# Kernel tuning notes

Hardware: AMD Instinct MI355X
Metric: run time of the kernel (lower is better)

The kernel has to match this reference:

```python
import math
import jax, jax.numpy as jnp
import numpy as np

N_EMBD = 448
NUM_HEADS = 8


def setup_inputs() -> dict:
    key = jax.random.key(0)
    ks = jax.random.split(key, 6)
    B, T, C = 4, 2048, N_EMBD
    x = jax.random.normal(ks[0], (B, T, C), dtype=jnp.float32)
    # Linear weights stored as [in, out]; y = x @ W (bias-free for q/k/v).
    s = 1.0 / math.sqrt(C)
    Wq = jax.random.normal(ks[1], (C, C), dtype=jnp.float32) * s
    Wk = jax.random.normal(ks[2], (C, C), dtype=jnp.float32) * s
    Wv = jax.random.normal(ks[3], (C, C), dtype=jnp.float32) * s
    Wp = jax.random.normal(ks[4], (C, C), dtype=jnp.float32) * s
    bp = jax.random.normal(ks[5], (C,), dtype=jnp.float32) * 0.01
    return {"x": x, "Wq": Wq, "Wk": Wk, "Wv": Wv, "Wp": Wp, "bp": bp}


def reference(x, Wq, Wk, Wv, Wp, bp):
    B, T, C = x.shape
    H = NUM_HEADS
    d = C // H
    # Projections, split into heads: [B, H, T, d]
    q = (x @ Wq).reshape(B, T, H, d).transpose(0, 2, 1, 3)
    k = (x @ Wk).reshape(B, T, H, d).transpose(0, 2, 1, 3)
    v = (x @ Wv).reshape(B, T, H, d).transpose(0, 2, 1, 3)
    # NOTE: original scales by 1/sqrt(C) (full embed dim), not 1/sqrt(head_dim).
    scale = 1.0 / math.sqrt(C)
    wei = jnp.einsum("bhtd,bhsd->bhts", q, k) * scale  # [B, H, T, T]
    causal = jnp.tril(jnp.ones((T, T), dtype=bool))
    wei = jnp.where(causal, wei, -jnp.inf)
    wei = jax.nn.softmax(wei, axis=-1)
    # dropout(p=0.2) is identity in eval mode
    out = jnp.einsum("bhts,bhsd->bhtd", wei, v)  # [B, H, T, d]
    out = out.transpose(0, 2, 1, 3).reshape(B, T, C)
    return out @ Wp + bp
```

## Files before the change

kernel.cpp:

```cpp
#include <hip/hip_runtime.h>
#include <math.h>

#define NB 4
#define NT 2048
#define NC 448
#define NH 8
#define ND 56
#define NM (NB * NT)
#define SCALE 0.04724555912615705f

typedef __attribute__((ext_vector_type(8))) short bf16x8;
typedef __attribute__((ext_vector_type(4))) float f32x4;

__device__ __forceinline__ unsigned short f2bf(float f) {
    unsigned u = __float_as_uint(f);
    u += 0x7fffu + ((u >> 16) & 1u);
    return (unsigned short)(u >> 16);
}
__device__ __forceinline__ float bf2f(unsigned short h) {
    return __uint_as_float(((unsigned)h) << 16);
}

__device__ __forceinline__ void gl_lds16(const unsigned short* g, unsigned short* l) {
    __builtin_amdgcn_global_load_lds(
        (const __attribute__((address_space(1))) unsigned int*)g,
        (__attribute__((address_space(3))) unsigned int*)l,
        16, 0, 0);
}

__device__ __forceinline__ int sw_slot(int row, int u) {
    return row * 4 + (u ^ ((row >> 1) & 3));
}

__global__ __launch_bounds__(256) void conv_x_kernel(
    const float* __restrict__ x, unsigned short* __restrict__ xh,
    unsigned short* __restrict__ xl)
{
    const size_t i4 = ((size_t)blockIdx.x * 256 + threadIdx.x) * 4;
    const float4 v = *reinterpret_cast<const float4*>(x + i4);
    ushort4 h, l;
    h.x = f2bf(v.x); l.x = f2bf(v.x - bf2f(h.x));
    h.y = f2bf(v.y); l.y = f2bf(v.y - bf2f(h.y));
    h.z = f2bf(v.z); l.z = f2bf(v.z - bf2f(h.z));
    h.w = f2bf(v.w); l.w = f2bf(v.w - bf2f(h.w));
    *reinterpret_cast<ushort4*>(xh + i4) = h;
    *reinterpret_cast<ushort4*>(xl + i4) = l;
}

__global__ __launch_bounds__(256) void conv_wt_kernel(
    const float* __restrict__ Wq, const float* __restrict__ Wk,
    const float* __restrict__ Wv, const float* __restrict__ Wp,
    unsigned short* __restrict__ wth, unsigned short* __restrict__ wtl)
{
    const int z = blockIdx.z;
    const float* __restrict__ W =
        (z == 0) ? Wq : ((z == 1) ? Wk : ((z == 2) ? Wv : Wp));
    unsigned short* __restrict__ oh = wth + (size_t)z * NC * NC;
    unsigned short* __restrict__ ol = wtl + (size_t)z * NC * NC;

    __shared__ float t[32][33];
    const int tx = threadIdx.x & 31;
    const int ty = threadIdx.x >> 5;
    const int x0 = blockIdx.x * 32;
    const int y0 = blockIdx.y * 32;

    #pragma unroll
    for (int i = 0; i < 4; ++i)
        t[ty + i * 8][tx] = W[(size_t)(y0 + ty + i * 8) * NC + x0 + tx];
    __syncthreads();
    #pragma unroll
    for (int i = 0; i < 4; ++i) {
        const int n = x0 + ty + i * 8;
        const int k = y0 + tx;
        const float v = t[tx][ty + i * 8];
        const unsigned short h = f2bf(v);
        oh[(size_t)n * NC + k] = h;
        ol[(size_t)n * NC + k] = f2bf(v - bf2f(h));
    }
}

__global__ __launch_bounds__(256) void qkv_mfma_kernel(
    const unsigned short* __restrict__ xh, const unsigned short* __restrict__ xl,
    const unsigned short* __restrict__ wth, const unsigned short* __restrict__ wtl,
    unsigned short* __restrict__ qo, unsigned short* __restrict__ ko,
    unsigned short* __restrict__ vo)
{
    const int z = blockIdx.z;
    const unsigned short* __restrict__ BTH = wth + (size_t)z * NC * NC;
    const unsigned short* __restrict__ BTL = wtl + (size_t)z * NC * NC;

    __shared__ unsigned short Ah[128 * 32], Al[128 * 32];
    __shared__ unsigned short Bh[64 * 32],  Bl[64 * 32];
    const int tid = threadIdx.x;
    const int l  = tid & 63, w = tid >> 6;
    const int lg = l >> 4,  lr = l & 15;
    const int wr = w >> 1,  wc = w & 1;
    const int rowBase = blockIdx.y * 128;
    const int colBase = blockIdx.x * 64;

    f32x4 acc[4][2];
    #pragma unroll
    for (int m = 0; m < 4; ++m)
        #pragma unroll
        for (int n = 0; n < 2; ++n) acc[m][n] = (f32x4){0.f, 0.f, 0.f, 0.f};

    for (int k0 = 0; k0 < NC; k0 += 32) {
        __syncthreads();
        #pragma unroll
        for (int i = 0; i < 2; ++i) {
            const int p   = w * 64 + 256 * i + l;
            const int row = p >> 2, ps = p & 3;
            const int u   = ps ^ ((row >> 1) & 3);
            const size_t src = (size_t)(rowBase + row) * NC + k0 + u * 8;
            const int dst = (w * 64 + 256 * i) * 8;
            gl_lds16(xh + src, Ah + dst);
            gl_lds16(xl + src, Al + dst);
        }
        {
            const int p   = w * 64 + l;
            const int row = p >> 2, ps = p & 3;
            const int u   = ps ^ ((row >> 1) & 3);
            const size_t src = (size_t)(colBase + row) * NC + k0 + u * 8;
            gl_lds16(BTH + src, Bh + w * 512);
            gl_lds16(BTL + src, Bl + w * 512);
        }
        __syncthreads();

        bf16x8 a_h[4], a_l[4], b_h[2], b_l[2];
        #pragma unroll
        for (int m = 0; m < 4; ++m) {
            const int row = wr * 64 + m * 16 + lr;
            const int s   = sw_slot(row, lg) * 8;
            a_h[m] = *reinterpret_cast<const bf16x8*>(Ah + s);
            a_l[m] = *reinterpret_cast<const bf16x8*>(Al + s);
        }
        #pragma unroll
        for (int n = 0; n < 2; ++n) {
            const int row = wc * 32 + n * 16 + lr;
            const int s   = sw_slot(row, lg) * 8;
            b_h[n] = *reinterpret_cast<const bf16x8*>(Bh + s);
            b_l[n] = *reinterpret_cast<const bf16x8*>(Bl + s);
        }
        #pragma unroll
        for (int m = 0; m < 4; ++m)
            #pragma unroll
            for (int n = 0; n < 2; ++n) {
                acc[m][n] = __builtin_amdgcn_mfma_f32_16x16x32_bf16(
                    a_h[m], b_h[n], acc[m][n], 0, 0, 0);
                acc[m][n] = __builtin_amdgcn_mfma_f32_16x16x32_bf16(
                    a_h[m], b_l[n], acc[m][n], 0, 0, 0);
                acc[m][n] = __builtin_amdgcn_mfma_f32_16x16x32_bf16(
                    a_l[m], b_h[n], acc[m][n], 0, 0, 0);
            }
    }

    const int mW = rowBase + wr * 64;
    const int nW = colBase + wc * 32;
    if (z < 2) {
        unsigned short* __restrict__ dst = (z == 0) ? qo : ko;
        #pragma unroll
        for (int m = 0; m < 4; ++m) {
            #pragma unroll
            for (int n = 0; n < 2; ++n) {
                const int gcol = nW + n * 16 + lr;
                const int h = gcol / ND, c = gcol - h * ND;
                #pragma unroll
                for (int r = 0; r < 4; ++r) {
                    const int grow = mW + m * 16 + lg * 4 + r;
                    const int b = grow >> 11, t = grow & (NT - 1);
                    dst[((size_t)(b * NH + h) * NT + t) * ND + c] =
                        f2bf(acc[m][n][r]);
                }
            }
        }
    } else {
        #pragma unroll
        for (int m = 0; m < 4; ++m) {
            const int grow0 = mW + m * 16 + lg * 4;
            const int b = grow0 >> 11, t0 = grow0 & (NT - 1);
            #pragma unroll
            for (int n = 0; n < 2; ++n) {
                const int gcol = nW + n * 16 + lr;
                const int h = gcol / ND, c = gcol - h * ND;
                ushort4 pk;
                pk.x = f2bf(acc[m][n][0]); pk.y = f2bf(acc[m][n][1]);
                pk.z = f2bf(acc[m][n][2]); pk.w = f2bf(acc[m][n][3]);
                *reinterpret_cast<ushort4*>(
                    vo + ((size_t)(b * NH + h) * ND + c) * NT + t0) = pk;
            }
        }
    }
}

__global__ __launch_bounds__(256) void proj_mfma_kernel(
    const unsigned short* __restrict__ ah_g, const unsigned short* __restrict__ al_g,
    const unsigned short* __restrict__ bth, const unsigned short* __restrict__ btl,
    const float* __restrict__ bias, float* __restrict__ out)
{
    __shared__ unsigned short Ah[128 * 32], Al[128 * 32];
    __shared__ unsigned short Bh[64 * 32],  Bl[64 * 32];
    const int tid = threadIdx.x;
    const int l  = tid & 63, w = tid >> 6;
    const int lg = l >> 4,  lr = l & 15;
    const int wr = w >> 1,  wc = w & 1;
    const int rowBase = blockIdx.y * 128;
    const int colBase = blockIdx.x * 64;

    f32x4 acc[4][2];
    #pragma unroll
    for (int m = 0; m < 4; ++m)
        #pragma unroll
        for (int n = 0; n < 2; ++n) acc[m][n] = (f32x4){0.f, 0.f, 0.f, 0.f};

    for (int k0 = 0; k0 < NC; k0 += 32) {
        __syncthreads();
        #pragma unroll
        for (int i = 0; i < 2; ++i) {
            const int p   = w * 64 + 256 * i + l;
            const int row = p >> 2, ps = p & 3;
            const int u   = ps ^ ((row >> 1) & 3);
            const size_t src = (size_t)(rowBase + row) * NC + k0 + u * 8;
            const int dst = (w * 64 + 256 * i) * 8;
            gl_lds16(ah_g + src, Ah + dst);
            gl_lds16(al_g + src, Al + dst);
        }
        {
            const int p   = w * 64 + l;
            const int row = p >> 2, ps = p & 3;
            const int u   = ps ^ ((row >> 1) & 3);
            const size_t src = (size_t)(colBase + row) * NC + k0 + u * 8;
            gl_lds16(bth + src, Bh + w * 512);
            gl_lds16(btl + src, Bl + w * 512);
        }
        __syncthreads();

        bf16x8 a_h[4], a_l[4], b_h[2], b_l[2];
        #pragma unroll
        for (int m = 0; m < 4; ++m) {
            const int row = wr * 64 + m * 16 + lr;
            const int s   = sw_slot(row, lg) * 8;
            a_h[m] = *reinterpret_cast<const bf16x8*>(Ah + s);
            a_l[m] = *reinterpret_cast<const bf16x8*>(Al + s);
        }
        #pragma unroll
        for (int n = 0; n < 2; ++n) {
            const int row = wc * 32 + n * 16 + lr;
            const int s   = sw_slot(row, lg) * 8;
            b_h[n] = *reinterpret_cast<const bf16x8*>(Bh + s);
            b_l[n] = *reinterpret_cast<const bf16x8*>(Bl + s);
        }
        #pragma unroll
        for (int m = 0; m < 4; ++m)
            #pragma unroll
            for (int n = 0; n < 2; ++n) {
                acc[m][n] = __builtin_amdgcn_mfma_f32_16x16x32_bf16(
                    a_h[m], b_h[n], acc[m][n], 0, 0, 0);
                acc[m][n] = __builtin_amdgcn_mfma_f32_16x16x32_bf16(
                    a_h[m], b_l[n], acc[m][n], 0, 0, 0);
                acc[m][n] = __builtin_amdgcn_mfma_f32_16x16x32_bf16(
                    a_l[m], b_h[n], acc[m][n], 0, 0, 0);
            }
    }

    const int mW = rowBase + wr * 64;
    const int nW = colBase + wc * 32;
    #pragma unroll
    for (int n = 0; n < 2; ++n) {
        const int gcol = nW + n * 16 + lr;
        const float bv = bias[gcol];
        #pragma unroll
        for (int m = 0; m < 4; ++m) {
            #pragma unroll
            for (int r = 0; r < 4; ++r) {
                const int grow = mW + m * 16 + lg * 4 + r;
                out[(size_t)grow * NC + gcol] = acc[m][n][r] + bv;
            }
        }
    }
}

__global__ __launch_bounds__(256) void attn_mfma_kernel(
    const unsigned short* __restrict__ q, const unsigned short* __restrict__ k,
    const unsigned short* __restrict__ vt,
    unsigned short* __restrict__ att_h, unsigned short* __restrict__ att_l)
{
    const int bh = blockIdx.x;
    const int qb = (gridDim.y - 1 - blockIdx.y) * 64;
    const int b  = bh >> 3;
    const int h  = bh & 7;

    const int tid = threadIdx.x;
    const int w   = tid >> 6;
    const int l   = tid & 63;
    const int lg  = l >> 4;
    const int lr  = l & 15;

    __shared__ unsigned short Ks [2][64 * 64];
    __shared__ unsigned short Vts[2][64 * 64];
    __shared__ unsigned short Pl[4][16 * 64];

    const unsigned short* __restrict__ Qg = q  + (size_t)bh * NT * ND;
    const unsigned short* __restrict__ Kg = k  + (size_t)bh * NT * ND;
    const unsigned short* __restrict__ Vg = vt + (size_t)bh * ND * NT;

    bf16x8 qf[2];
    {
        const int row = qb + w * 16 + lr;
        #pragma unroll
        for (int hh = 0; hh < 2; ++hh) {
            const int d0 = hh * 32 + lg * 8;
            bf16x8 tmp = {0, 0, 0, 0, 0, 0, 0, 0};
            if (d0 < ND)
                tmp = *reinterpret_cast<const bf16x8*>(Qg + (size_t)row * ND + d0);
            qf[hh] = tmp;
        }
    }

    const f32x4 fzero = {0.f, 0.f, 0.f, 0.f};
    f32x4 o[4];
    #pragma unroll
    for (int n = 0; n < 4; ++n) o[n] = fzero;
    float mrun[4] = {-INFINITY, -INFINITY, -INFINITY, -INFINITY};
    float lrun[4] = {0.f, 0.f, 0.f, 0.f};

    uint4 rK[2][2], rV[2][2];
    #pragma unroll
    for (int s = 0; s < 2; ++s)
        #pragma unroll
        for (int cc = 0; cc < 2; ++cc) {
            const int ch = tid + cc * 256;
            const int row = ch >> 3, u = ch & 7;
            uint4 kvv = make_uint4(0u, 0u, 0u, 0u);
            uint4 vvv = make_uint4(0u, 0u, 0u, 0u);
            if (u < 7)
                kvv = *reinterpret_cast<const uint4*>(
                    Kg + (size_t)(s * 64 + row) * ND + u * 8);
            if (row < ND)
                vvv = *reinterpret_cast<const uint4*>(
                    Vg + (size_t)row * NT + s * 64 + u * 8);
            rK[s][cc] = kvv; rV[s][cc] = vvv;
        }

    for (int kb = 0; kb <= qb; kb += 128) {
        #pragma unroll
        for (int s = 0; s < 2; ++s)
            #pragma unroll
            for (int cc = 0; cc < 2; ++cc) {
                const int ch = tid + cc * 256;
                const int row = ch >> 3, u = ch & 7;
                const int sl = (row * 8 + (u ^ (row & 7))) * 8;
                *reinterpret_cast<uint4*>(&Ks[s][sl])  = rK[s][cc];
                *reinterpret_cast<uint4*>(&Vts[s][sl]) = rV[s][cc];
            }
        __syncthreads();

        if (kb + 128 <= qb) {
            #pragma unroll
            for (int s = 0; s < 2; ++s)
                #pragma unroll
                for (int cc = 0; cc < 2; ++cc) {
                    const int ch = tid + cc * 256;
                    const int row = ch >> 3, u = ch & 7;
                    uint4 kvv = make_uint4(0u, 0u, 0u, 0u);
                    uint4 vvv = make_uint4(0u, 0u, 0u, 0u);
                    if (u < 7)
                        kvv = *reinterpret_cast<const uint4*>(
                            Kg + (size_t)(kb + 128 + s * 64 + row) * ND + u * 8);
                    if (row < ND)
                        vvv = *reinterpret_cast<const uint4*>(
                            Vg + (size_t)row * NT + kb + 128 + s * 64 + u * 8);
                    rK[s][cc] = kvv; rV[s][cc] = vvv;
                }
        }

        f32x4 sc[2][4];
        __builtin_amdgcn_s_setprio(1);
        #pragma unroll
        for (int s = 0; s < 2; ++s)
            #pragma unroll
            for (int n = 0; n < 4; ++n) {
                const int krow = n * 16 + lr;
                const bf16x8 kf0 = *reinterpret_cast<const bf16x8*>(
                    &Ks[s][(krow * 8 + ((0 + lg) ^ (krow & 7))) * 8]);
                const bf16x8 kf1 = *reinterpret_cast<const bf16x8*>(
                    &Ks[s][(krow * 8 + ((4 + lg) ^ (krow & 7))) * 8]);
                f32x4 a = fzero;
                a = __builtin_amdgcn_mfma_f32_16x16x32_bf16(qf[0], kf0, a, 0, 0, 0);
                a = __builtin_amdgcn_mfma_f32_16x16x32_bf16(qf[1], kf1, a, 0, 0, 0);
                sc[s][n] = a;
            }
        __builtin_amdgcn_s_setprio(0);

        #pragma unroll
        for (int s = 0; s < 2; ++s) {
            const int kbs = kb + s * 64;
            if (kbs + 63 > qb) {
                #pragma unroll
                for (int n = 0; n < 4; ++n) {
                    const int key = kbs + n * 16 + lr;
                    #pragma unroll
                    for (int r = 0; r < 4; ++r) {
                        const int qr = qb + w * 16 + lg * 4 + r;
                        if (key > qr) sc[s][n][r] = -1e30f;
                    }
                }
            }
        }

        float alpha[4];
        #pragma unroll
        for (int r = 0; r < 4; ++r) {
            float tmax = fmaxf(
                fmaxf(fmaxf(sc[0][0][r], sc[0][1][r]), fmaxf(sc[0][2][r], sc[0][3][r])),
                fmaxf(fmaxf(sc[1][0][r], sc[1][1][r]), fmaxf(sc[1][2][r], sc[1][3][r])));
            tmax = fmaxf(tmax, __shfl_xor(tmax, 1));
            tmax = fmaxf(tmax, __shfl_xor(tmax, 2));
            tmax = fmaxf(tmax, __shfl_xor(tmax, 4));
            tmax = fmaxf(tmax, __shfl_xor(tmax, 8));
            const float mnew = fmaxf(mrun[r], tmax);
            const float c = SCALE * mnew;
            alpha[r] = __expf(fmaf(SCALE, mrun[r], -c));
            mrun[r]  = mnew;
            float tsum = 0.f;
            #pragma unroll
            for (int s = 0; s < 2; ++s)
                #pragma unroll
                for (int n = 0; n < 4; ++n) {
                    const float p = __expf(fmaf(SCALE, sc[s][n][r], -c));
                    sc[s][n][r] = p;
                    tsum += p;
                }
            tsum += __shfl_xor(tsum, 1);
            tsum += __shfl_xor(tsum, 2);
            tsum += __shfl_xor(tsum, 4);
            tsum += __shfl_xor(tsum, 8);
            lrun[r] = lrun[r] * alpha[r] + tsum;
        }
        #pragma unroll
        for (int n = 0; n < 4; ++n)
            #pragma unroll
            for (int r = 0; r < 4; ++r) o[n][r] *= alpha[r];

        unsigned short* Pw = Pl[w];
        #pragma unroll
        for (int s = 0; s < 2; ++s) {
            #pragma unroll
            for (int n = 0; n < 4; ++n) {
                const int u = n * 2 + (lr >> 3);
                #pragma unroll
                for (int r = 0; r < 4; ++r) {
                    const int prow = lg * 4 + r;
                    Pw[(prow * 8 + (u ^ (prow & 7))) * 8 + (lr & 7)] =
                        f2bf(sc[s][n][r]);
                }
            }
            const bf16x8 pf0 = *reinterpret_cast<const bf16x8*>(
                &Pw[(lr * 8 + ((0 + lg) ^ (lr & 7))) * 8]);
            const bf16x8 pf1 = *reinterpret_cast<const bf16x8*>(
                &Pw[(lr * 8 + ((4 + lg) ^ (lr & 7))) * 8]);
            __builtin_amdgcn_s_setprio(1);
            #pragma unroll
            for (int n = 0; n < 4; ++n) {
                const int vrow = n * 16 + lr;
                const bf16x8 vf0 = *reinterpret_cast<const bf16x8*>(
                    &Vts[s][(vrow * 8 + ((0 + lg) ^ (vrow & 7))) * 8]);
                const bf16x8 vf1 = *reinterpret_cast<const bf16x8*>(
                    &Vts[s][(vrow * 8 + ((4 + lg) ^ (vrow & 7))) * 8]);
                o[n] = __builtin_amdgcn_mfma_f32_16x16x32_bf16(pf0, vf0, o[n], 0, 0, 0);
                o[n] = __builtin_amdgcn_mfma_f32_16x16x32_bf16(pf1, vf1, o[n], 0, 0, 0);
            }
            __builtin_amdgcn_s_setprio(0);
        }
        __syncthreads();
    }

    #pragma unroll
    for (int r = 0; r < 4; ++r) {
        const float inv = 1.0f / lrun[r];
        const int trow = qb + w * 16 + lg * 4 + r;
        const size_t rbase = ((size_t)b * NT + trow) * NC + h * ND;
        #pragma unroll
        for (int n = 0; n < 4; ++n) {
            const int c = n * 16 + lr;
            if (c < ND) {
                const float val = o[n][r] * inv;
                const unsigned short hh = f2bf(val);
                att_h[rbase + c] = hh;
                att_l[rbase + c] = f2bf(val - bf2f(hh));
            }
        }
    }
}

extern "C" void kernel_launch(void* const* d_in, const int* in_sizes, int n_in,
                              void* d_out, int out_size, void* d_ws, size_t ws_size,
                              hipStream_t stream)
{
    const float* x  = (const float*)d_in[0];
    const float* Wq = (const float*)d_in[1];
    const float* Wk = (const float*)d_in[2];
    const float* Wv = (const float*)d_in[3];
    const float* Wp = (const float*)d_in[4];
    const float* bp = (const float*)d_in[5];
    float* out = (float*)d_out;

    const size_t BTC = (size_t)NM * NC;
    const size_t WSZ = (size_t)NC * NC;
    unsigned short* p = (unsigned short*)d_ws;
    unsigned short* xh  = p;            p += BTC;
    unsigned short* xl  = p;            p += BTC;
    unsigned short* wth = p;            p += 4 * WSZ;
    unsigned short* wtl = p;            p += 4 * WSZ;
    unsigned short* qw  = p;            p += BTC;
    unsigned short* kw  = p;            p += BTC;
    unsigned short* vtw = p;            p += BTC;
    unsigned short* ath = p;            p += BTC;
    unsigned short* atl = p;            p += BTC;

    dim3 blk(256);
    conv_x_kernel<<<dim3((unsigned)(BTC / 1024)), blk, 0, stream>>>(x, xh, xl);
    conv_wt_kernel<<<dim3(NC / 32, NC / 32, 4), blk, 0, stream>>>(
        Wq, Wk, Wv, Wp, wth, wtl);
    qkv_mfma_kernel<<<dim3(NC / 64, NM / 128, 3), blk, 0, stream>>>(
        xh, xl, wth, wtl, qw, kw, vtw);
    attn_mfma_kernel<<<dim3(NB * NH, NT / 64), blk, 0, stream>>>(
        qw, kw, vtw, ath, atl);
    proj_mfma_kernel<<<dim3(NC / 64, NM / 128, 1), blk, 0, stream>>>(
        ath, atl, wth + 3 * WSZ, wtl + 3 * WSZ, bp, out);
}
```

Baseline: 226.8 us.

## Fuse Q, K, V projections into one block sharing the loaded x tile

The QKV GEMM kernel now computes all three projections in a single block instead of launching a z-dimension of three. Each x tile (hi and lo parts) is loaded into LDS once and reused against three weight tiles, cutting global and LDS traffic for x by a factor of three. The cost is three times the accumulator registers (96 floats per lane) and larger LDS use, which may lower occupancy. The grid also shrinks to a third of the blocks, leaving fewer blocks to spread across the CUs.

```diff
diff --git a/kernel.cpp b/kernel.cpp
--- a/kernel.cpp
+++ b/kernel.cpp
@@ -85,12 +85,8 @@
     unsigned short* __restrict__ qo, unsigned short* __restrict__ ko,
     unsigned short* __restrict__ vo)
 {
-    const int z = blockIdx.z;
-    const unsigned short* __restrict__ BTH = wth + (size_t)z * NC * NC;
-    const unsigned short* __restrict__ BTL = wtl + (size_t)z * NC * NC;
-
     __shared__ unsigned short Ah[128 * 32], Al[128 * 32];
-    __shared__ unsigned short Bh[64 * 32],  Bl[64 * 32];
+    __shared__ unsigned short Bh[3][64 * 32], Bl[3][64 * 32];
     const int tid = threadIdx.x;
     const int l  = tid & 63, w = tid >> 6;
     const int lg = l >> 4,  lr = l & 15;
@@ -98,11 +94,13 @@
     const int rowBase = blockIdx.y * 128;
     const int colBase = blockIdx.x * 64;
 
-    f32x4 acc[4][2];
-    #pragma unroll
-    for (int m = 0; m < 4; ++m)
-        #pragma unroll
-        for (int n = 0; n < 2; ++n) acc[m][n] = (f32x4){0.f, 0.f, 0.f, 0.f};
+    f32x4 acc[3][4][2];
+    #pragma unroll
+    for (int z = 0; z < 3; ++z)
+        #pragma unroll
+        for (int m = 0; m < 4; ++m)
+            #pragma unroll
+            for (int n = 0; n < 2; ++n) acc[z][m][n] = (f32x4){0.f, 0.f, 0.f, 0.f};
 
     for (int k0 = 0; k0 < NC; k0 += 32) {
         __syncthreads();
@@ -117,16 +115,20 @@
             gl_lds16(xl + src, Al + dst);
         }
         {
-            const int p   = w * 64 + l;
+            const int p   = tid;
             const int row = p >> 2, ps = p & 3;
             const int u   = ps ^ ((row >> 1) & 3);
-            const size_t src = (size_t)(colBase + row) * NC + k0 + u * 8;
-            gl_lds16(BTH + src, Bh + w * 512);
-            gl_lds16(BTL + src, Bl + w * 512);
+            const size_t off = (size_t)(colBase + row) * NC + k0 + u * 8;
+            #pragma unroll
+            for (int z = 0; z < 3; ++z) {
+                const size_t src = (size_t)z * NC * NC + off;
+                gl_lds16(wth + src, &Bh[z][w * 512]);
+                gl_lds16(wtl + src, &Bl[z][w * 512]);
+            }
         }
         __syncthreads();
 
-        bf16x8 a_h[4], a_l[4], b_h[2], b_l[2];
+        bf16x8 a_h[4], a_l[4];
         #pragma unroll
         for (int m = 0; m < 4; ++m) {
             const int row = wr * 64 + m * 16 + lr;
@@ -135,58 +137,65 @@
             a_l[m] = *reinterpret_cast<const bf16x8*>(Al + s);
         }
         #pragma unroll
-        for (int n = 0; n < 2; ++n) {
-            const int row = wc * 32 + n * 16 + lr;
-            const int s   = sw_slot(row, lg) * 8;
-            b_h[n] = *reinterpret_cast<const bf16x8*>(Bh + s);
-            b_l[n] = *reinterpret_cast<const bf16x8*>(Bl + s);
-        }
-        #pragma unroll
-        for (int m = 0; m < 4; ++m)
+        for (int z = 0; z < 3; ++z) {
+            bf16x8 b_h[2], b_l[2];
             #pragma unroll
             for (int n = 0; n < 2; ++n) {
-                acc[m][n] = __builtin_amdgcn_mfma_f32_16x16x32_bf16(
-                    a_h[m], b_h[n], acc[m][n], 0, 0, 0);
-                acc[m][n] = __builtin_amdgcn_mfma_f32_16x16x32_bf16(
-                    a_h[m], b_l[n], acc[m][n], 0, 0, 0);
-                acc[m][n] = __builtin_amdgcn_mfma_f32_16x16x32_bf16(
-                    a_l[m], b_h[n], acc[m][n], 0, 0, 0);
-            }
+                const int row = wc * 32 + n * 16 + lr;
+                const int s   = sw_slot(row, lg) * 8;
+                b_h[n] = *reinterpret_cast<const bf16x8*>(&Bh[z][s]);
+                b_l[n] = *reinterpret_cast<const bf16x8*>(&Bl[z][s]);
+            }
+            #pragma unroll
+            for (int m = 0; m < 4; ++m)
+                #pragma unroll
+                for (int n = 0; n < 2; ++n) {
+                    acc[z][m][n] = __builtin_amdgcn_mfma_f32_16x16x32_bf16(
+                        a_h[m], b_h[n], acc[z][m][n], 0, 0, 0);
+                    acc[z][m][n] = __builtin_amdgcn_mfma_f32_16x16x32_bf16(
+                        a_h[m], b_l[n], acc[z][m][n], 0, 0, 0);
+                    acc[z][m][n] = __builtin_amdgcn_mfma_f32_16x16x32_bf16(
+                        a_l[m], b_h[n], acc[z][m][n], 0, 0, 0);
+                }
+        }
     }
 
     const int mW = rowBase + wr * 64;
     const int nW = colBase + wc * 32;
-    if (z < 2) {
-        unsigned short* __restrict__ dst = (z == 0) ? qo : ko;
-        #pragma unroll
-        for (int m = 0; m < 4; ++m) {
-            #pragma unroll
-            for (int n = 0; n < 2; ++n) {
-                const int gcol = nW + n * 16 + lr;
-                const int h = gcol / ND, c = gcol - h * ND;
-                #pragma unroll
-                for (int r = 0; r < 4; ++r) {
-                    const int grow = mW + m * 16 + lg * 4 + r;
-                    const int b = grow >> 11, t = grow & (NT - 1);
-                    dst[((size_t)(b * NH + h) * NT + t) * ND + c] =
-                        f2bf(acc[m][n][r]);
-                }
-            }
-        }
-    } else {
-        #pragma unroll
-        for (int m = 0; m < 4; ++m) {
-            const int grow0 = mW + m * 16 + lg * 4;
-            const int b = grow0 >> 11, t0 = grow0 & (NT - 1);
-            #pragma unroll
-            for (int n = 0; n < 2; ++n) {
-                const int gcol = nW + n * 16 + lr;
-                const int h = gcol / ND, c = gcol - h * ND;
-                ushort4 pk;
-                pk.x = f2bf(acc[m][n][0]); pk.y = f2bf(acc[m][n][1]);
-                pk.z = f2bf(acc[m][n][2]); pk.w = f2bf(acc[m][n][3]);
-                *reinterpret_cast<ushort4*>(
-                    vo + ((size_t)(b * NH + h) * ND + c) * NT + t0) = pk;
+    #pragma unroll
+    for (int z = 0; z < 3; ++z) {
+        if (z < 2) {
+            unsigned short* __restrict__ dst = (z == 0) ? qo : ko;
+            #pragma unroll
+            for (int m = 0; m < 4; ++m) {
+                #pragma unroll
+                for (int n = 0; n < 2; ++n) {
+                    const int gcol = nW + n * 16 + lr;
+                    const int h = gcol / ND, c = gcol - h * ND;
+                    #pragma unroll
+                    for (int r = 0; r < 4; ++r) {
+                        const int grow = mW + m * 16 + lg * 4 + r;
+                        const int b = grow >> 11, t = grow & (NT - 1);
+                        dst[((size_t)(b * NH + h) * NT + t) * ND + c] =
+                            f2bf(acc[z][m][n][r]);
+                    }
+                }
+            }
+        } else {
+            #pragma unroll
+            for (int m = 0; m < 4; ++m) {
+                const int grow0 = mW + m * 16 + lg * 4;
+                const int b = grow0 >> 11, t0 = grow0 & (NT - 1);
+                #pragma unroll
+                for (int n = 0; n < 2; ++n) {
+                    const int gcol = nW + n * 16 + lr;
+                    const int h = gcol / ND, c = gcol - h * ND;
+                    ushort4 pk;
+                    pk.x = f2bf(acc[z][m][n][0]); pk.y = f2bf(acc[z][m][n][1]);
+                    pk.z = f2bf(acc[z][m][n][2]); pk.w = f2bf(acc[z][m][n][3]);
+                    *reinterpret_cast<ushort4*>(
+                        vo + ((size_t)(b * NH + h) * ND + c) * NT + t0) = pk;
+                }
             }
         }
     }
@@ -521,7 +530,7 @@
     conv_x_kernel<<<dim3((unsigned)(BTC / 1024)), blk, 0, stream>>>(x, xh, xl);
     conv_wt_kernel<<<dim3(NC / 32, NC / 32, 4), blk, 0, stream>>>(
         Wq, Wk, Wv, Wp, wth, wtl);
-    qkv_mfma_kernel<<<dim3(NC / 64, NM / 128, 3), blk, 0, stream>>>(
+    qkv_mfma_kernel<<<dim3(NC / 64, NM / 128), blk, 0, stream>>>(
         xh, xl, wth, wtl, qw, kw, vtw);
     attn_mfma_kernel<<<dim3(NB * NH, NT / 64), blk, 0, stream>>>(
         qw, kw, vtw, ath, atl);
```

After: 215.8 us. 4.8% less time.
